# Kernel tuning notes

Hardware: AMD Instinct MI355X
Metric: run time of the kernel (lower is better)

Reference implementation:

```python
import jax, jax.numpy as jnp
import numpy as np

B, S, D = 4, 2048, 1024
H = 4 * D          # expert hidden dim
E_SPEC = 4         # num specific experts
E_SHR = 2          # num shared experts
TOP_K = 2


def setup_inputs() -> dict:
    key = jax.random.key(0)
    ks = jax.random.split(key, 16)
    s = 0.02
    return {
        "x": jax.random.normal(ks[0], (B, S, D), jnp.float32),
        # specific experts (stacked over expert axis)
        "spec_w1": jax.random.normal(ks[1], (E_SPEC, D, H), jnp.float32) * s,
        "spec_b1": jnp.zeros((E_SPEC, H), jnp.float32),
        "spec_w2": jax.random.normal(ks[2], (E_SPEC, H, D), jnp.float32) * s,
        "spec_b2": jnp.zeros((E_SPEC, D), jnp.float32),
        "spec_rw": jax.random.normal(ks[3], (D, E_SPEC), jnp.float32) * s,
        "spec_rb": jnp.zeros((E_SPEC,), jnp.float32),
        # shared experts
        "shr_w1": jax.random.normal(ks[4], (E_SHR, D, H), jnp.float32) * s,
        "shr_b1": jnp.zeros((E_SHR, H), jnp.float32),
        "shr_w2": jax.random.normal(ks[5], (E_SHR, H, D), jnp.float32) * s,
        "shr_b2": jnp.zeros((E_SHR, D), jnp.float32),
        "shr_rw": jax.random.normal(ks[6], (D, E_SHR), jnp.float32) * s,
        "shr_rb": jnp.zeros((E_SHR,), jnp.float32),
    }


def _expert_mlp(xf, w1, b1, w2, b2):
    # xf: [T, D]; w1: [E, D, H]; w2: [E, H, D] -> [E, T, D]
    h = jax.nn.gelu(jnp.einsum("td,edh->eth", xf, w1) + b1[:, None, :],
                    approximate=False)
    return jnp.einsum("eth,ehd->etd", h, w2) + b2[:, None, :]


def reference(x, spec_w1, spec_b1, spec_w2, spec_b2, spec_rw, spec_rb,
              shr_w1, shr_b1, shr_w2, shr_b2, shr_rw, shr_rb):
    b, s, d = x.shape
    xf = x.reshape(-1, d)                      # [T, D]
    T = xf.shape[0]

    # --- specific (top-k) routing ---
    spec_probs = jax.nn.softmax(xf @ spec_rw + spec_rb, axis=-1)   # [T, E]
    topk_probs, topk_idx = jax.lax.top_k(spec_probs, TOP_K)        # [T, K]

    # aux load-balancing loss
    counts = jnp.zeros((E_SPEC,), jnp.float32).at[topk_idx.reshape(-1)].add(1.0)
    fraction = counts / (T * TOP_K)
    aux_loss = E_SPEC * jnp.sum(fraction * spec_probs.mean(axis=0))

    # gate[t, e] = sum_k topk_probs[t,k] * 1[topk_idx[t,k]==e]
    gate = jnp.sum(jax.nn.one_hot(topk_idx, E_SPEC, dtype=xf.dtype)
                   * topk_probs[..., None], axis=1)                # [T, E]

    spec_out_e = _expert_mlp(xf, spec_w1, spec_b1, spec_w2, spec_b2)  # [E, T, D]
    specific_out = jnp.einsum("te,etd->td", gate, spec_out_e)

    # --- shared (dense) experts ---
    shr_probs = jax.nn.softmax(xf @ shr_rw + shr_rb, axis=-1)      # [T, E_shr]
    shr_out_e = _expert_mlp(xf, shr_w1, shr_b1, shr_w2, shr_b2)    # [E_shr, T, D]
    shared_out = jnp.einsum("te,etd->td", shr_probs, shr_out_e)

    final = (specific_out + shared_out).reshape(b, s, d)
    return final, aux_loss
```

## Files before the change

kernel.cpp:

```cpp
#include <hip/hip_runtime.h>
#include <hip/hip_bf16.h>

#define T_TOK 8192
#define DDIM 1024
#define HDIM 4096

typedef __bf16 bf16;
typedef bf16 bf16x8 __attribute__((ext_vector_type(8)));
typedef float f32x4 __attribute__((ext_vector_type(4)));

#define ASM_VMCNT(n) asm volatile("s_waitcnt vmcnt(" #n ")" ::: "memory")
#define MFMA16(a, b, c) __builtin_amdgcn_mfma_f32_16x16x32_bf16((a), (b), (c), 0, 0, 0)

__device__ __forceinline__ void gl_lds16(const void* g, void* l) {
  __builtin_amdgcn_global_load_lds(
      (const __attribute__((address_space(1))) unsigned int*)g,
      (__attribute__((address_space(3))) unsigned int*)l, 16, 0, 0);
}

__device__ __forceinline__ float gelu_f(float v) {
  const float x = v * 0.7071067811865475f;
  const float ax = fabsf(x);
  const float t = 1.0f / fmaf(0.3275911f, ax, 1.0f);
  float p = fmaf(1.061405429f, t, -1.453152027f);
  p = fmaf(p, t, 1.421413741f);
  p = fmaf(p, t, -0.284496736f);
  p = fmaf(p, t, 0.254829592f);
  p = p * t;
  const float e = __expf(-ax * ax);
  const float er = fmaf(-p, e, 1.0f);
  const float erfx = (x >= 0.0f) ? er : -er;
  return 0.5f * v * (1.0f + erfx);
}

__global__ __launch_bounds__(256) void conv_router(
    const float* __restrict__ x, bf16* __restrict__ xb,
    const float* __restrict__ srw, const float* __restrict__ srb,
    const float* __restrict__ hrw, const float* __restrict__ hrb,
    float* __restrict__ gate, float4* __restrict__ probs4,
    int* __restrict__ top2) {
  const int lane = threadIdx.x & 63;
  const int w = threadIdx.x >> 6;
  const int t = blockIdx.x * 4 + w;

  const float* xr = x + (size_t)t * DDIM;
  bf16* xbr = xb + (size_t)t * DDIM;
  float p0 = 0, p1 = 0, p2 = 0, p3 = 0, p4 = 0, p5 = 0;
#pragma unroll
  for (int c = 0; c < 4; ++c) {
    const int d = c * 256 + lane * 4;
    const float4 xv = *(const float4*)(xr + d);
    bf16 ov[4] = {(bf16)xv.x, (bf16)xv.y, (bf16)xv.z, (bf16)xv.w};
    *(float2*)(xbr + d) = *(float2*)ov;
    const float xa[4] = {xv.x, xv.y, xv.z, xv.w};
#pragma unroll
    for (int j = 0; j < 4; ++j) {
      const float xd = xa[j];
      const float4 r4 = *(const float4*)(srw + (size_t)(d + j) * 4);
      p0 += xd * r4.x; p1 += xd * r4.y; p2 += xd * r4.z; p3 += xd * r4.w;
      const float2 r2 = *(const float2*)(hrw + (size_t)(d + j) * 2);
      p4 += xd * r2.x; p5 += xd * r2.y;
    }
  }
#pragma unroll
  for (int off = 32; off >= 1; off >>= 1) {
    p0 += __shfl_xor(p0, off);
    p1 += __shfl_xor(p1, off);
    p2 += __shfl_xor(p2, off);
    p3 += __shfl_xor(p3, off);
    p4 += __shfl_xor(p4, off);
    p5 += __shfl_xor(p5, off);
  }
  if (lane == 0) {
    const float l0 = p0 + srb[0], l1 = p1 + srb[1];
    const float l2 = p2 + srb[2], l3 = p3 + srb[3];
    const float m = fmaxf(fmaxf(l0, l1), fmaxf(l2, l3));
    const float e0 = expf(l0 - m), e1 = expf(l1 - m);
    const float e2 = expf(l2 - m), e3 = expf(l3 - m);
    const float s = e0 + e1 + e2 + e3;
    float pr[4] = {e0 / s, e1 / s, e2 / s, e3 / s};
    int i1 = 0; float v1 = pr[0];
#pragma unroll
    for (int e = 1; e < 4; ++e) if (pr[e] > v1) { v1 = pr[e]; i1 = e; }
    int i2 = -1; float v2 = -1.0f;
#pragma unroll
    for (int e = 0; e < 4; ++e)
      if (e != i1 && pr[e] > v2) { v2 = pr[e]; i2 = e; }
    float g[4] = {0, 0, 0, 0};
    g[i1] = v1; g[i2] = v2;
    float* gr = gate + (size_t)t * 8;
    gr[0] = g[0]; gr[1] = g[1]; gr[2] = g[2]; gr[3] = g[3];
    const float h0 = p4 + hrb[0], h1 = p5 + hrb[1];
    const float mh = fmaxf(h0, h1);
    const float q0 = expf(h0 - mh), q1 = expf(h1 - mh);
    const float qs = q0 + q1;
    gr[4] = q0 / qs; gr[5] = q1 / qs; gr[6] = 0; gr[7] = 0;
    probs4[t] = make_float4(pr[0], pr[1], pr[2], pr[3]);
    top2[t] = i1 | (i2 << 8);
  }
}

__global__ __launch_bounds__(256) void transpose_convert6(
    const float* __restrict__ spec_w, const float* __restrict__ shr_w,
    bf16* __restrict__ dst, int R, int C) {
  __shared__ float tile[32][33];
  const int z = blockIdx.z;
  const float* src = (z < 4) ? spec_w + (size_t)z * R * C
                             : shr_w + (size_t)(z - 4) * R * C;
  bf16* d = dst + (size_t)z * R * C;
  const int c0 = blockIdx.x * 32, r0 = blockIdx.y * 32;
  const int tx = threadIdx.x & 31, ty = threadIdx.x >> 5;
#pragma unroll
  for (int i = 0; i < 4; ++i)
    tile[ty + 8 * i][tx] = src[(size_t)(r0 + ty + 8 * i) * C + c0 + tx];
  __syncthreads();
#pragma unroll
  for (int i = 0; i < 4; ++i)
    d[(size_t)(c0 + ty + 8 * i) * R + r0 + tx] = (bf16)tile[tx][ty + 8 * i];
}

__global__ __launch_bounds__(1024) void scan_build(
    const int* __restrict__ top2, const float4* __restrict__ probs4,
    int* __restrict__ meta, int* __restrict__ lists,
    float* __restrict__ auxg) {
  __shared__ unsigned long long sc[1024];
  __shared__ float4 rp[512];
  const int tid = threadIdx.x;

  int ee[8];
  unsigned long long c = 0;
  float4 ps = make_float4(0.f, 0.f, 0.f, 0.f);
#pragma unroll
  for (int j = 0; j < 8; ++j) {
    const int t = tid * 8 + j;
    const int p = top2[t];
    ee[j] = p;
    const int a = p & 15, b = (p >> 8) & 15;
    c += (1ULL << (16 * a)) + (1ULL << (16 * b));
    const float4 pv = probs4[t];
    ps.x += pv.x; ps.y += pv.y; ps.z += pv.z; ps.w += pv.w;
  }
  sc[tid] = c;
  __syncthreads();
  for (int off = 1; off < 1024; off <<= 1) {
    const unsigned long long mine = sc[tid];
    const unsigned long long prev = (tid >= off) ? sc[tid - off] : 0ULL;
    __syncthreads();
    sc[tid] = mine + prev;
    __syncthreads();
  }
  const unsigned long long incl = sc[tid];
  const unsigned long long tot = sc[1023];
  const unsigned long long excl = incl - c;
  int q0 = (int)(excl & 0xffff), q1 = (int)((excl >> 16) & 0xffff);
  int q2 = (int)((excl >> 32) & 0xffff), q3 = (int)((excl >> 48) & 0xffff);
#pragma unroll
  for (int j = 0; j < 8; ++j) {
    const int t = tid * 8 + j;
    const int a = ee[j] & 15, b = (ee[j] >> 8) & 15;
    const int pa = (a == 0) ? q0 : (a == 1) ? q1 : (a == 2) ? q2 : q3;
    lists[a * 8192 + pa] = t;
    q0 += (a == 0); q1 += (a == 1); q2 += (a == 2); q3 += (a == 3);
    const int pb = (b == 0) ? q0 : (b == 1) ? q1 : (b == 2) ? q2 : q3;
    lists[b * 8192 + pb] = t;
    q0 += (b == 0); q1 += (b == 1); q2 += (b == 2); q3 += (b == 3);
  }
  if (tid == 1023) {
    const int c0 = (int)(tot & 0xffff), c1 = (int)((tot >> 16) & 0xffff);
    const int c2 = (int)((tot >> 32) & 0xffff), c3 = (int)((tot >> 48) & 0xffff);
    meta[24] = c0; meta[25] = c1; meta[26] = c2; meta[27] = c3;
    auxg[0] = (float)c0; auxg[1] = (float)c1;
    auxg[2] = (float)c2; auxg[3] = (float)c3;
    const int nb0 = (c0 + 255) >> 8, nb1 = (c1 + 255) >> 8;
    const int nb2 = (c2 + 255) >> 8, nb3 = (c3 + 255) >> 8;
    const int ch0 = (nb0 + 3) >> 2, ch1 = (nb1 + 3) >> 2;
    const int ch2 = (nb2 + 3) >> 2, ch3 = (nb3 + 3) >> 2;
    meta[28] = 0;
    meta[29] = 128 * ch0;
    meta[30] = meta[29] + 128 * ch1;
    meta[31] = meta[30] + 128 * ch2;
    meta[32] = meta[31] + 128 * ch3;
    meta[34] = 0;
    meta[35] = nb0 * 256;
    meta[36] = meta[35] + nb1 * 256;
    meta[37] = meta[36] + nb2 * 256;
  }
  if (tid >= 512) rp[tid - 512] = ps;
  __syncthreads();
  if (tid < 512) {
    const float4 o = rp[tid];
    ps.x += o.x; ps.y += o.y; ps.z += o.z; ps.w += o.w;
  }
  for (int w = 256; w >= 1; w >>= 1) {
    __syncthreads();
    if (tid >= w && tid < 2 * w) rp[tid - w] = ps;
    __syncthreads();
    if (tid < w) {
      const float4 o = rp[tid];
      ps.x += o.x; ps.y += o.y; ps.z += o.z; ps.w += o.w;
    }
  }
  if (tid == 0) {
    auxg[4] = ps.x; auxg[5] = ps.y; auxg[6] = ps.z; auxg[7] = ps.w;
  }
}

__global__ void aux_finalize(const float* __restrict__ auxg,
                             float* __restrict__ outp) {
  float a = 0.0f;
#pragma unroll
  for (int e = 0; e < 4; ++e)
    a += (auxg[e] / (float)(T_TOK * 2)) * (auxg[4 + e] / (float)T_TOK);
  outp[0] = 4.0f * a;
}

template <int KIND>
__global__ __launch_bounds__(256, 2) void g1k(
    const bf16* __restrict__ A, const bf16* __restrict__ B,
    const float* __restrict__ bias, bf16* __restrict__ h_all, int N,
    int NCN, int CH_M, int CH_N, const int* __restrict__ meta,
    const int* __restrict__ lists, int e) {
  __shared__ __align__(1024) bf16 As[3 * 256 * 32];
  __shared__ __align__(1024) bf16 Bs[3 * 128 * 32];

  const int tid = threadIdx.x;
  const int lane = tid & 63, wid = tid >> 6;
  const int wm = wid >> 1, wn = wid & 1;
  const int lr = lane & 15, lg = lane >> 4;

  int bm, bn, hb = 0, s = e;
  const bf16* Bp = B;
  const float* biasp = bias;
  if constexpr (KIND == 0) {
    const int xcd = blockIdx.x & 7, idx = blockIdx.x >> 3;
    bm = (xcd / NCN) * CH_M + idx / CH_N;
    bn = (xcd % NCN) * CH_N + idx % CH_N;
  } else if constexpr (KIND == 1) {
    const int b = blockIdx.x;
    if (b >= meta[32]) return;
    s = (b >= meta[29]) + (b >= meta[30]) + (b >= meta[31]);
    const int local = b - meta[28 + s];
    const int nbm = (meta[24 + s] + 255) >> 8;
    const int CHm = (nbm + 3) >> 2;
    if (local >= 8 * CHm * 16) return;
    const int xc = local & 7, idx = local >> 3;
    bm = (xc >> 1) * CHm + idx / 16;
    bn = (xc & 1) * 16 + idx % 16;
    if (bm >= nbm) return;
    hb = meta[34 + s];
    Bp = B + (size_t)s * DDIM * HDIM;
    biasp = bias + (size_t)s * HDIM;
  } else {
    const int nbm = (meta[24 + e] + 255) >> 8;
    const int CHm = (nbm + 3) >> 2;
    if (blockIdx.x >= 8 * CHm * 16) return;
    const int xc = blockIdx.x & 7, idx = blockIdx.x >> 3;
    bm = (xc >> 1) * CHm + idx / 16;
    bn = (xc & 1) * 16 + idx % 16;
    if (bm >= nbm) return;
  }
  const int K = DDIM;

  const int rl = tid >> 2;
  const int c = ((tid & 3) * 16) ^ (((rl >> 1) & 3) << 4);
  int ar0 = bm * 256 + rl, ar1 = ar0 + 64, ar2 = ar0 + 128, ar3 = ar0 + 192;
  if constexpr (KIND != 0) {
    const int* lp = lists + s * 8192;
    int t;
    t = lp[ar0]; ar0 = t < 0 ? 0 : t;
    t = lp[ar1]; ar1 = t < 0 ? 0 : t;
    t = lp[ar2]; ar2 = t < 0 ? 0 : t;
    t = lp[ar3]; ar3 = t < 0 ? 0 : t;
  }
  const bf16* sA0 = A + (size_t)ar0 * K + (c >> 1);
  const bf16* sA1 = A + (size_t)ar1 * K + (c >> 1);
  const bf16* sA2 = A + (size_t)ar2 * K + (c >> 1);
  const bf16* sA3 = A + (size_t)ar3 * K + (c >> 1);
  const bf16* sB0 = Bp + (size_t)(bn * 128 + rl) * K + (c >> 1);
  const bf16* sB1 = Bp + (size_t)(bn * 128 + 64 + rl) * K + (c >> 1);

  char* const dA = (char*)As + wid * 1024;
  char* const dB = (char*)Bs + wid * 1024;

  const int rkey = ((lr >> 1) & 3) << 4;
  const char* Ard = (const char*)As + (wm * 128 + lr) * 64 + ((lg * 16) ^ rkey);
  const char* Brd = (const char*)Bs + (wn * 64 + lr) * 64 + ((lg * 16) ^ rkey);

  f32x4 acc[8][4] = {};
  const int NT = K >> 5;

#define GW_STAGE(KO, SLOT)                         \
  gl_lds16(sA0 + (KO), dA + (SLOT)*16384);         \
  gl_lds16(sA1 + (KO), dA + (SLOT)*16384 + 4096);  \
  gl_lds16(sA2 + (KO), dA + (SLOT)*16384 + 8192);  \
  gl_lds16(sA3 + (KO), dA + (SLOT)*16384 + 12288); \
  gl_lds16(sB0 + (KO), dB + (SLOT)*8192);          \
  gl_lds16(sB1 + (KO), dB + (SLOT)*8192 + 4096);
  GW_STAGE(0, 0)
  GW_STAGE(32, 1)
  GW_STAGE(64, 2)
  ASM_VMCNT(12);
  __builtin_amdgcn_s_barrier();

#define GW_ITER(KT, SLOT)                                                  \
  {                                                                        \
    bf16x8 af[8], bfr[4];                                                  \
    _Pragma("unroll") for (int mf = 0; mf < 8; ++mf)                       \
        af[mf] = *(const bf16x8*)(Ard + (SLOT)*16384 + mf * 1024);         \
    _Pragma("unroll") for (int nf = 0; nf < 4; ++nf)                       \
        bfr[nf] = *(const bf16x8*)(Brd + (SLOT)*8192 + nf * 1024);         \
    asm volatile("s_waitcnt lgkmcnt(0)" ::: "memory");                     \
    __builtin_amdgcn_s_setprio(1);                                         \
    _Pragma("unroll") for (int mf = 0; mf < 8; ++mf)                       \
        _Pragma("unroll") for (int nf = 0; nf < 4; ++nf)                   \
            acc[mf][nf] = MFMA16(af[mf], bfr[nf], acc[mf][nf]);            \
    __builtin_amdgcn_s_setprio(0);                                         \
    __builtin_amdgcn_s_barrier();                                          \
    if ((KT) + 3 < NT) {                                                   \
      const int ko_ = ((KT) + 3) << 5;                                     \
      GW_STAGE(ko_, SLOT)                                                  \
      ASM_VMCNT(12);                                                       \
    } else if ((KT) + 2 < NT) {                                            \
      ASM_VMCNT(6);                                                        \
    } else if ((KT) + 1 < NT) {                                            \
      ASM_VMCNT(0);                                                        \
    }                                                                      \
    __builtin_amdgcn_s_barrier();                                          \
  }

  for (int kt0 = 0; kt0 < NT; kt0 += 3) {
    GW_ITER(kt0, 0)
    if (kt0 + 1 < NT) GW_ITER(kt0 + 1, 1)
    if (kt0 + 2 < NT) GW_ITER(kt0 + 2, 2)
  }

  const int colb = bn * 128 + wn * 64;
  const int rowb = hb + bm * 256 + wm * 128 + lg * 4;
  float bv[4];
#pragma unroll
  for (int nf = 0; nf < 4; ++nf) bv[nf] = biasp[colb + nf * 16 + lr];
#pragma unroll
  for (int mf = 0; mf < 8; ++mf)
#pragma unroll
    for (int nf = 0; nf < 4; ++nf) {
      const int col = colb + nf * 16 + lr;
#pragma unroll
      for (int r = 0; r < 4; ++r) {
        const int row = rowb + mf * 16 + r;
        h_all[(size_t)row * N + col] = (bf16)gelu_f(acc[mf][nf][r] + bv[nf]);
      }
    }
}

template <int EMODE>
__global__ __launch_bounds__(512, 2) void g2k(
    const bf16* __restrict__ A, int lda, const bf16* __restrict__ B,
    const float* __restrict__ bias, float* __restrict__ out,
    const float* __restrict__ gate, int gidx, const int* __restrict__ meta,
    const int* __restrict__ lists, int e, int packed) {
  __shared__ __align__(1024) bf16 Alds[2 * 256 * 64];
  __shared__ __align__(1024) bf16 Blds[2 * 128 * 64];

  const int tid = threadIdx.x;
  const int lane = tid & 63, wid = tid >> 6;
  const int wm = wid >> 2, wn = wid & 3;
  const int lr = lane & 15, lg = lane >> 4;

  int bm, bn, hb = 0;
  if constexpr (EMODE == 3) {
    const int nbm = (meta[24 + e] + 255) >> 8;
    const int CHm = (nbm + 3) >> 2;
    if (blockIdx.x >= 8 * CHm * 4) return;
    const int xc = blockIdx.x & 7, idx = blockIdx.x >> 3;
    bm = (xc >> 1) * CHm + idx / 4;
    bn = (xc & 1) * 4 + idx % 4;
    if (bm >= nbm) return;
    hb = packed ? meta[34 + e] : 0;
  } else {
    const int xcd = blockIdx.x & 7, idx = blockIdx.x >> 3;
    bm = (xcd >> 1) * 8 + idx / 4;
    bn = (xcd & 1) * 4 + idx % 4;
  }
  const int K = HDIM, N = DDIM;
  const int NT = K >> 6;

  const int L = tid * 16;
  const int rl = L >> 7;
  const int colb = (L & 127) ^ ((rl & 7) << 4);

  const int ar0 = hb + bm * 256 + rl;
  const bf16* sAc0 = A + (size_t)ar0 * lda + (colb >> 1);
  const bf16* sAc1 = A + (size_t)(ar0 + 64) * lda + (colb >> 1);
  const bf16* sAc2 = A + (size_t)(ar0 + 128) * lda + (colb >> 1);
  const bf16* sAc3 = A + (size_t)(ar0 + 192) * lda + (colb >> 1);
  const bf16* sB = B + (size_t)(bn * 128 + rl) * K + (colb >> 1);

  char* const ldsA = (char*)Alds;
  char* const ldsB = (char*)Blds;
  const int wb = wid * 1024;
  char* const stA[2] = {ldsA + wb, ldsA + 32768 + wb};
  char* const stB[2] = {ldsB + wb, ldsB + 16384 + wb};

  const int ax0 = (lg * 16) ^ ((lr & 7) << 4);
  const int ax1 = ax0 ^ 64;
  const int aro = (wm * 128 + lr) * 128;
  const int bro = (wn * 32 + lr) * 128;
  const char* const Ak0[2] = {ldsA + aro + ax0, ldsA + 32768 + aro + ax0};
  const char* const Ak1[2] = {ldsA + aro + ax1, ldsA + 32768 + aro + ax1};
  const char* const Bk0[2] = {ldsB + bro + ax0, ldsB + 16384 + bro + ax0};
  const char* const Bk1[2] = {ldsB + bro + ax1, ldsB + 16384 + bro + ax1};

  f32x4 acc[8][2] = {};

  gl_lds16(sAc0, stA[0]);
  gl_lds16(sAc1, stA[0] + 8192);
  gl_lds16(sAc2, stA[0] + 16384);
  gl_lds16(sAc3, stA[0] + 24576);
  gl_lds16(sB, stB[0]);
  gl_lds16(sB + (size_t)64 * K, stB[0] + 8192);
  gl_lds16(sB + 64, stB[1]);
  gl_lds16(sB + (size_t)64 * K + 64, stB[1] + 8192);
  gl_lds16(sAc0 + 64, stA[1]);
  gl_lds16(sAc1 + 64, stA[1] + 8192);
  ASM_VMCNT(4);
  __builtin_amdgcn_s_barrier();

  for (int kt0 = 0; kt0 < NT; kt0 += 2) {
#pragma unroll
    for (int par = 0; par < 2; ++par) {
      const int kt = kt0 + par;
      const int cur = par, oth = par ^ 1;
      const bool st1 = (kt + 1) < NT, st2 = (kt + 2) < NT;
      const size_t ko1 = (size_t)(kt + 1) << 6, ko2 = (size_t)(kt + 2) << 6;
      const char* Ac0 = Ak0[cur]; const char* Ac1 = Ak1[cur];
      const char* Bc0 = Bk0[cur]; const char* Bc1 = Bk1[cur];

      bf16x8 af[4][2], bfr[2][2];

#pragma unroll
      for (int mf = 0; mf < 4; ++mf) {
        af[mf][0] = *(const bf16x8*)(Ac0 + mf * 2048);
        af[mf][1] = *(const bf16x8*)(Ac1 + mf * 2048);
      }
      bfr[0][0] = *(const bf16x8*)(Bc0);
      bfr[0][1] = *(const bf16x8*)(Bc1);
      if (st1) {
        gl_lds16(sAc2 + ko1, stA[oth] + 16384);
        gl_lds16(sAc3 + ko1, stA[oth] + 24576);
      }
      __builtin_amdgcn_s_barrier();
      asm volatile("s_waitcnt lgkmcnt(0)" ::: "memory");
      __builtin_amdgcn_sched_barrier(0);
      __builtin_amdgcn_s_setprio(1);
#pragma unroll
      for (int mf = 0; mf < 4; ++mf) {
        acc[mf][0] = MFMA16(af[mf][0], bfr[0][0], acc[mf][0]);
        acc[mf][0] = MFMA16(af[mf][1], bfr[0][1], acc[mf][0]);
      }
      __builtin_amdgcn_s_setprio(0);
      __builtin_amdgcn_s_barrier();

      bfr[1][0] = *(const bf16x8*)(Bc0 + 2048);
      bfr[1][1] = *(const bf16x8*)(Bc1 + 2048);
      __builtin_amdgcn_s_barrier();
      asm volatile("s_waitcnt lgkmcnt(0)" ::: "memory");
      __builtin_amdgcn_sched_barrier(0);
      __builtin_amdgcn_s_setprio(1);
#pragma unroll
      for (int mf = 0; mf < 4; ++mf) {
        acc[mf][1] = MFMA16(af[mf][0], bfr[1][0], acc[mf][1]);
        acc[mf][1] = MFMA16(af[mf][1], bfr[1][1], acc[mf][1]);
      }
      __builtin_amdgcn_s_setprio(0);
      __builtin_amdgcn_s_barrier();

#pragma unroll
      for (int mf = 0; mf < 4; ++mf) {
        af[mf][0] = *(const bf16x8*)(Ac0 + 8192 + mf * 2048);
        af[mf][1] = *(const bf16x8*)(Ac1 + 8192 + mf * 2048);
      }
      if (st2) {
        gl_lds16(sB + ko2, stB[cur]);
        gl_lds16(sB + (size_t)64 * K + ko2, stB[cur] + 8192);
      }
      __builtin_amdgcn_s_barrier();
      asm volatile("s_waitcnt lgkmcnt(0)" ::: "memory");
      __builtin_amdgcn_sched_barrier(0);
      __builtin_amdgcn_s_setprio(1);
#pragma unroll
      for (int mf = 0; mf < 4; ++mf) {
        acc[4 + mf][0] = MFMA16(af[mf][0], bfr[0][0], acc[4 + mf][0]);
        acc[4 + mf][0] = MFMA16(af[mf][1], bfr[0][1], acc[4 + mf][0]);
      }
      __builtin_amdgcn_s_setprio(0);
      __builtin_amdgcn_s_barrier();

      if (st2) {
        gl_lds16(sAc0 + ko2, stA[cur]);
        gl_lds16(sAc1 + ko2, stA[cur] + 8192);
      }
      __builtin_amdgcn_s_setprio(1);
#pragma unroll
      for (int mf = 0; mf < 4; ++mf) {
        acc[4 + mf][1] = MFMA16(af[mf][0], bfr[1][0], acc[4 + mf][1]);
        acc[4 + mf][1] = MFMA16(af[mf][1], bfr[1][1], acc[4 + mf][1]);
      }
      __builtin_amdgcn_s_setprio(0);
      if (st2) {
        ASM_VMCNT(4);
        __builtin_amdgcn_s_barrier();
      } else if (st1) {
        ASM_VMCNT(0);
        __builtin_amdgcn_s_barrier();
      }
    }
  }

  const int colb2 = bn * 128 + wn * 32;
  const int rowb = bm * 256 + wm * 128 + lg * 4;
  float bv[2];
#pragma unroll
  for (int nf = 0; nf < 2; ++nf) bv[nf] = bias[colb2 + nf * 16 + lr];
#pragma unroll
  for (int mf = 0; mf < 8; ++mf) {
    if constexpr (EMODE != 3) {
      float gv[4];
#pragma unroll
      for (int r = 0; r < 4; ++r)
        gv[r] = gate[(size_t)(rowb + mf * 16 + r) * 8 + gidx];
#pragma unroll
      for (int nf = 0; nf < 2; ++nf) {
        const int col = colb2 + nf * 16 + lr;
#pragma unroll
        for (int r = 0; r < 4; ++r) {
          const float v = acc[mf][nf][r] + bv[nf];
          const size_t oi = (size_t)(rowb + mf * 16 + r) * N + col;
          if constexpr (EMODE == 1)
            out[oi] += gv[r] * v;
          else
            out[oi] = gv[r] * v;
        }
      }
    } else {
      const int* lp = lists + e * 8192;
      int tok[4]; float gv[4];
#pragma unroll
      for (int r = 0; r < 4; ++r) {
        tok[r] = lp[rowb + mf * 16 + r];
        gv[r] = tok[r] >= 0 ? gate[(size_t)tok[r] * 8 + gidx] : 0.0f;
      }
#pragma unroll
      for (int nf = 0; nf < 2; ++nf) {
        const int col = colb2 + nf * 16 + lr;
#pragma unroll
        for (int r = 0; r < 4; ++r) {
          if (tok[r] >= 0) {
            const float v = acc[mf][nf][r] + bv[nf];
            out[(size_t)tok[r] * N + col] += gv[r] * v;
          }
        }
      }
    }
  }
}

extern "C" void kernel_launch(void* const* d_in, const int* in_sizes, int n_in,
                              void* d_out, int out_size, void* d_ws,
                              size_t ws_size, hipStream_t stream) {
  const float* x = (const float*)d_in[0];
  const float* spec_w1 = (const float*)d_in[1];
  const float* spec_b1 = (const float*)d_in[2];
  const float* spec_w2 = (const float*)d_in[3];
  const float* spec_b2 = (const float*)d_in[4];
  const float* spec_rw = (const float*)d_in[5];
  const float* spec_rb = (const float*)d_in[6];
  const float* shr_w1 = (const float*)d_in[7];
  const float* shr_b1 = (const float*)d_in[8];
  const float* shr_w2 = (const float*)d_in[9];
  const float* shr_b2 = (const float*)d_in[10];
  const float* shr_rw = (const float*)d_in[11];
  const float* shr_rb = (const float*)d_in[12];
  float* out = (float*)d_out;

  char* ws = (char*)d_ws;
  const size_t DH = (size_t)DDIM * HDIM;
  const size_t OFF_W1 = 16777216;
  const size_t OFF_W2 = OFF_W1 + 50331648;
  const size_t OFF_GATE = OFF_W2 + 50331648;
  const size_t OFF_AUX = OFF_GATE + 262144;
  const size_t OFF_META = OFF_AUX + 256;
  const size_t OFF_LIST = OFF_META + 256;
  const size_t OFF_T2 = OFF_LIST + 131072;
  const size_t OFF_P4 = OFF_T2 + 32768;
  const size_t OFF_H = OFF_P4 + 131072 + 1024;
  bf16* xb = (bf16*)ws;
  bf16* w1t = (bf16*)(ws + OFF_W1);
  bf16* w2t = (bf16*)(ws + OFF_W2);
  float* gate = (float*)(ws + OFF_GATE);
  float* auxg = (float*)(ws + OFF_AUX);
  int* meta = (int*)(ws + OFF_META);
  int* lists = (int*)(ws + OFF_LIST);
  int* top2 = (int*)(ws + OFF_T2);
  float4* probs4 = (float4*)(ws + OFF_P4);
  bf16* h = (bf16*)(ws + OFF_H);

  const bool rich = ws_size >= OFF_H + (size_t)17408 * HDIM * 2;

  hipMemsetAsync(lists, 0xFF, 4 * 8192 * 4, stream);

  conv_router<<<T_TOK / 4, 256, 0, stream>>>(x, xb, spec_rw, spec_rb, shr_rw,
                                             shr_rb, gate, probs4, top2);
  scan_build<<<1, 1024, 0, stream>>>(top2, probs4, meta, lists, auxg);

  transpose_convert6<<<dim3(HDIM / 32, DDIM / 32, 6), 256, 0, stream>>>(
      spec_w1, shr_w1, w1t, DDIM, HDIM);
  transpose_convert6<<<dim3(DDIM / 32, HDIM / 32, 6), 256, 0, stream>>>(
      spec_w2, shr_w2, w2t, HDIM, DDIM);

  if (rich) {
    g1k<0><<<2048, 256, 0, stream>>>(xb, w1t + 4 * DH, shr_b1, h, 8192,
                                     4, 16, 16, meta, lists, 0);
    g2k<0><<<256, 512, 0, stream>>>(h, 8192, w2t + 4 * DH, shr_b2, out,
                                    gate, 4, meta, lists, 0, 0);
    g2k<1><<<256, 512, 0, stream>>>(h + 4096, 8192, w2t + 5 * DH,
                                    shr_b2 + 1024, out, gate, 5, meta,
                                    lists, 0, 0);
    g1k<1><<<4096, 256, 0, stream>>>(xb, w1t, spec_b1, h, 4096,
                                     2, 8, 16, meta, lists, 0);
    for (int e = 0; e < 4; ++e)
      g2k<3><<<256, 512, 0, stream>>>(h, 4096, w2t + (size_t)e * DH,
                                      spec_b2 + (size_t)e * DDIM, out, gate,
                                      e, meta, lists, e, 1);
  } else {
    for (int es = 0; es < 2; ++es) {
      g1k<0><<<1024, 256, 0, stream>>>(xb, w1t + (4 + es) * DH,
                                       shr_b1 + (size_t)es * HDIM, h, 4096,
                                       2, 8, 16, meta, lists, 0);
      if (es == 0)
        g2k<0><<<256, 512, 0, stream>>>(h, 4096, w2t + 4 * DH, shr_b2, out,
                                        gate, 4, meta, lists, 0, 0);
      else
        g2k<1><<<256, 512, 0, stream>>>(h, 4096, w2t + 5 * DH,
                                        shr_b2 + 1024, out, gate, 5, meta,
                                        lists, 0, 0);
    }
    for (int e = 0; e < 4; ++e) {
      g1k<2><<<1024, 256, 0, stream>>>(xb, w1t + (size_t)e * DH,
                                       spec_b1 + (size_t)e * HDIM, h, 4096,
                                       2, 8, 16, meta, lists, e);
      g2k<3><<<256, 512, 0, stream>>>(h, 4096, w2t + (size_t)e * DH,
                                      spec_b2 + (size_t)e * DDIM, out, gate,
                                      e, meta, lists, e, 0);
    }
  }
  aux_finalize<<<1, 1, 0, stream>>>(auxg, out + (size_t)T_TOK * DDIM);
}
```

Baseline: 1.019 ms.

## Replace first-layer GEMM with 256x256 tile, 8-wave, ping-pong pipelined kernel

The first expert GEMM kernel moves from a 256x128 tile with 4 waves and a 3-stage K=32 pipeline to a 256x256 tile with 8 waves, K=64 steps and two LDS buffers. Global-to-LDS loads are interleaved with MFMA phases under fine-grained barriers, and the LDS swizzle and block-to-XCD mapping are updated to match. The aim is higher arithmetic intensity per loaded byte and better overlap of loads with matrix math. The cost is larger LDS use (128 KB per block), which limits occupancy, plus many extra barriers per K step. Grid sizes and routing metadata offsets are rescaled for the new tile width.

```diff
diff --git a/kernel.cpp b/kernel.cpp
--- a/kernel.cpp
+++ b/kernel.cpp
@@ -11,6 +11,10 @@
 
 #define ASM_VMCNT(n) asm volatile("s_waitcnt vmcnt(" #n ")" ::: "memory")
 #define MFMA16(a, b, c) __builtin_amdgcn_mfma_f32_16x16x32_bf16((a), (b), (c), 0, 0, 0)
+#define G8_BAR __builtin_amdgcn_s_barrier()
+#define G8_WAIT                                            \
+  asm volatile("s_waitcnt lgkmcnt(0)" ::: "memory");       \
+  __builtin_amdgcn_sched_barrier(0)
 
 __device__ __forceinline__ void gl_lds16(const void* g, void* l) {
   __builtin_amdgcn_global_load_lds(
@@ -175,15 +179,15 @@
     const int nb2 = (c2 + 255) >> 8, nb3 = (c3 + 255) >> 8;
     const int ch0 = (nb0 + 3) >> 2, ch1 = (nb1 + 3) >> 2;
     const int ch2 = (nb2 + 3) >> 2, ch3 = (nb3 + 3) >> 2;
-    meta[28] = 0;
-    meta[29] = 128 * ch0;
-    meta[30] = meta[29] + 128 * ch1;
-    meta[31] = meta[30] + 128 * ch2;
-    meta[32] = meta[31] + 128 * ch3;
     meta[34] = 0;
     meta[35] = nb0 * 256;
     meta[36] = meta[35] + nb1 * 256;
     meta[37] = meta[36] + nb2 * 256;
+    meta[40] = 0;
+    meta[41] = 64 * ch0;
+    meta[42] = meta[41] + 64 * ch1;
+    meta[43] = meta[42] + 64 * ch2;
+    meta[44] = meta[43] + 64 * ch3;
   }
   if (tid >= 512) rp[tid - 512] = ps;
   __syncthreads();
@@ -215,126 +219,172 @@
 }
 
 template <int KIND>
-__global__ __launch_bounds__(256, 2) void g1k(
-    const bf16* __restrict__ A, const bf16* __restrict__ B,
+__global__ __launch_bounds__(512, 2) void g8(
+    const bf16* __restrict__ A, const bf16* __restrict__ Bw,
     const float* __restrict__ bias, bf16* __restrict__ h_all, int N,
-    int NCN, int CH_M, int CH_N, const int* __restrict__ meta,
+    int CH_M, int CH_N, const int* __restrict__ meta,
     const int* __restrict__ lists, int e) {
-  __shared__ __align__(1024) bf16 As[3 * 256 * 32];
-  __shared__ __align__(1024) bf16 Bs[3 * 128 * 32];
+  __shared__ __align__(1024) bf16 Alds[2 * 256 * 64];
+  __shared__ __align__(1024) bf16 Blds[2 * 256 * 64];
 
   const int tid = threadIdx.x;
   const int lane = tid & 63, wid = tid >> 6;
-  const int wm = wid >> 1, wn = wid & 1;
+  const int wm = wid >> 2, wn = wid & 3;
   const int lr = lane & 15, lg = lane >> 4;
 
   int bm, bn, hb = 0, s = e;
-  const bf16* Bp = B;
+  const bf16* Bp = Bw;
   const float* biasp = bias;
   if constexpr (KIND == 0) {
     const int xcd = blockIdx.x & 7, idx = blockIdx.x >> 3;
-    bm = (xcd / NCN) * CH_M + idx / CH_N;
-    bn = (xcd % NCN) * CH_N + idx % CH_N;
+    bm = (xcd >> 1) * CH_M + idx / CH_N;
+    bn = (xcd & 1) * CH_N + idx % CH_N;
   } else if constexpr (KIND == 1) {
     const int b = blockIdx.x;
-    if (b >= meta[32]) return;
-    s = (b >= meta[29]) + (b >= meta[30]) + (b >= meta[31]);
-    const int local = b - meta[28 + s];
+    if (b >= meta[44]) return;
+    s = (b >= meta[41]) + (b >= meta[42]) + (b >= meta[43]);
+    const int local = b - meta[40 + s];
     const int nbm = (meta[24 + s] + 255) >> 8;
     const int CHm = (nbm + 3) >> 2;
-    if (local >= 8 * CHm * 16) return;
+    if (local >= 64 * CHm) return;
     const int xc = local & 7, idx = local >> 3;
-    bm = (xc >> 1) * CHm + idx / 16;
-    bn = (xc & 1) * 16 + idx % 16;
+    bm = (xc >> 1) * CHm + idx / 8;
+    bn = (xc & 1) * 8 + idx % 8;
     if (bm >= nbm) return;
     hb = meta[34 + s];
-    Bp = B + (size_t)s * DDIM * HDIM;
+    Bp = Bw + (size_t)s * DDIM * HDIM;
     biasp = bias + (size_t)s * HDIM;
   } else {
     const int nbm = (meta[24 + e] + 255) >> 8;
     const int CHm = (nbm + 3) >> 2;
-    if (blockIdx.x >= 8 * CHm * 16) return;
+    if (blockIdx.x >= 64 * CHm) return;
     const int xc = blockIdx.x & 7, idx = blockIdx.x >> 3;
-    bm = (xc >> 1) * CHm + idx / 16;
-    bn = (xc & 1) * 16 + idx % 16;
+    bm = (xc >> 1) * CHm + idx / 8;
+    bn = (xc & 1) * 8 + idx % 8;
     if (bm >= nbm) return;
   }
   const int K = DDIM;
-
-  const int rl = tid >> 2;
-  const int c = ((tid & 3) * 16) ^ (((rl >> 1) & 3) << 4);
-  int ar0 = bm * 256 + rl, ar1 = ar0 + 64, ar2 = ar0 + 128, ar3 = ar0 + 192;
+  const int NT = K >> 6;
+
+  const int rl = tid >> 3;
+  const int cbs = ((tid * 16) & 127) ^ ((rl & 7) << 4);
+  int ar[4];
+#pragma unroll
+  for (int c = 0; c < 4; ++c) ar[c] = bm * 256 + c * 64 + rl;
   if constexpr (KIND != 0) {
     const int* lp = lists + s * 8192;
-    int t;
-    t = lp[ar0]; ar0 = t < 0 ? 0 : t;
-    t = lp[ar1]; ar1 = t < 0 ? 0 : t;
-    t = lp[ar2]; ar2 = t < 0 ? 0 : t;
-    t = lp[ar3]; ar3 = t < 0 ? 0 : t;
-  }
-  const bf16* sA0 = A + (size_t)ar0 * K + (c >> 1);
-  const bf16* sA1 = A + (size_t)ar1 * K + (c >> 1);
-  const bf16* sA2 = A + (size_t)ar2 * K + (c >> 1);
-  const bf16* sA3 = A + (size_t)ar3 * K + (c >> 1);
-  const bf16* sB0 = Bp + (size_t)(bn * 128 + rl) * K + (c >> 1);
-  const bf16* sB1 = Bp + (size_t)(bn * 128 + 64 + rl) * K + (c >> 1);
-
-  char* const dA = (char*)As + wid * 1024;
-  char* const dB = (char*)Bs + wid * 1024;
-
-  const int rkey = ((lr >> 1) & 3) << 4;
-  const char* Ard = (const char*)As + (wm * 128 + lr) * 64 + ((lg * 16) ^ rkey);
-  const char* Brd = (const char*)Bs + (wn * 64 + lr) * 64 + ((lg * 16) ^ rkey);
+#pragma unroll
+    for (int c = 0; c < 4; ++c) {
+      const int t = lp[ar[c]];
+      ar[c] = t < 0 ? 0 : t;
+    }
+  }
+  const bf16* sA[4];
+  const bf16* sB[4];
+#pragma unroll
+  for (int c = 0; c < 4; ++c) {
+    sA[c] = A + (size_t)ar[c] * K + (cbs >> 1);
+    sB[c] = Bp + (size_t)(bn * 256 + c * 64 + rl) * K + (cbs >> 1);
+  }
+  char* const ldsA = (char*)Alds;
+  char* const ldsB = (char*)Blds;
+  const int wb = wid * 1024;
+
+  const int ax0 = (lg * 16) ^ ((lr & 7) << 4);
+  const int ax1 = ax0 ^ 64;
+  const int aro = (wm * 128 + lr) * 128;
+  const int bro = (wn * 64 + lr) * 128;
+  const char* const A0 = (const char*)Alds + aro + ax0;
+  const char* const A1 = (const char*)Alds + aro + ax1;
+  const char* const B0 = (const char*)Blds + bro + ax0;
+  const char* const B1 = (const char*)Blds + bro + ax1;
 
   f32x4 acc[8][4] = {};
-  const int NT = K >> 5;
-
-#define GW_STAGE(KO, SLOT)                         \
-  gl_lds16(sA0 + (KO), dA + (SLOT)*16384);         \
-  gl_lds16(sA1 + (KO), dA + (SLOT)*16384 + 4096);  \
-  gl_lds16(sA2 + (KO), dA + (SLOT)*16384 + 8192);  \
-  gl_lds16(sA3 + (KO), dA + (SLOT)*16384 + 12288); \
-  gl_lds16(sB0 + (KO), dB + (SLOT)*8192);          \
-  gl_lds16(sB1 + (KO), dB + (SLOT)*8192 + 4096);
-  GW_STAGE(0, 0)
-  GW_STAGE(32, 1)
-  GW_STAGE(64, 2)
-  ASM_VMCNT(12);
-  __builtin_amdgcn_s_barrier();
-
-#define GW_ITER(KT, SLOT)                                                  \
-  {                                                                        \
-    bf16x8 af[8], bfr[4];                                                  \
-    _Pragma("unroll") for (int mf = 0; mf < 8; ++mf)                       \
-        af[mf] = *(const bf16x8*)(Ard + (SLOT)*16384 + mf * 1024);         \
-    _Pragma("unroll") for (int nf = 0; nf < 4; ++nf)                       \
-        bfr[nf] = *(const bf16x8*)(Brd + (SLOT)*8192 + nf * 1024);         \
-    asm volatile("s_waitcnt lgkmcnt(0)" ::: "memory");                     \
-    __builtin_amdgcn_s_setprio(1);                                         \
-    _Pragma("unroll") for (int mf = 0; mf < 8; ++mf)                       \
-        _Pragma("unroll") for (int nf = 0; nf < 4; ++nf)                   \
-            acc[mf][nf] = MFMA16(af[mf], bfr[nf], acc[mf][nf]);            \
-    __builtin_amdgcn_s_setprio(0);                                         \
-    __builtin_amdgcn_s_barrier();                                          \
-    if ((KT) + 3 < NT) {                                                   \
-      const int ko_ = ((KT) + 3) << 5;                                     \
-      GW_STAGE(ko_, SLOT)                                                  \
-      ASM_VMCNT(12);                                                       \
-    } else if ((KT) + 2 < NT) {                                            \
-      ASM_VMCNT(6);                                                        \
-    } else if ((KT) + 1 < NT) {                                            \
-      ASM_VMCNT(0);                                                        \
-    }                                                                      \
-    __builtin_amdgcn_s_barrier();                                          \
-  }
-
-  for (int kt0 = 0; kt0 < NT; kt0 += 3) {
-    GW_ITER(kt0, 0)
-    if (kt0 + 1 < NT) GW_ITER(kt0 + 1, 1)
-    if (kt0 + 2 < NT) GW_ITER(kt0 + 2, 2)
-  }
-
-  const int colb = bn * 128 + wn * 64;
+  bf16x8 af[4][2], b01[2][2], b23[2][2];
+
+#define G8_RA(BOFF, MB)                                               \
+  _Pragma("unroll") for (int i = 0; i < 4; ++i) {                     \
+    af[i][0] = *(const bf16x8*)(A0 + (BOFF) + ((MB) + i) * 2048);     \
+    af[i][1] = *(const bf16x8*)(A1 + (BOFF) + ((MB) + i) * 2048);     \
+  }
+#define G8_RB(BOFF, DST, NB)                                          \
+  _Pragma("unroll") for (int i = 0; i < 2; ++i) {                     \
+    DST[i][0] = *(const bf16x8*)(B0 + (BOFF) + ((NB) + i) * 2048);    \
+    DST[i][1] = *(const bf16x8*)(B1 + (BOFF) + ((NB) + i) * 2048);    \
+  }
+#define G8_MMA(MB, NB, BSRC)                                          \
+  __builtin_amdgcn_s_setprio(1);                                      \
+  _Pragma("unroll") for (int i = 0; i < 4; ++i)                       \
+    _Pragma("unroll") for (int j = 0; j < 2; ++j) {                   \
+      acc[(MB) + i][(NB) + j] =                                       \
+          MFMA16(af[i][0], BSRC[j][0], acc[(MB) + i][(NB) + j]);      \
+      acc[(MB) + i][(NB) + j] =                                       \
+          MFMA16(af[i][1], BSRC[j][1], acc[(MB) + i][(NB) + j]);      \
+    }                                                                 \
+  __builtin_amdgcn_s_setprio(0);
+#define G8_STG_B(T, C, BUFO)                                          \
+  gl_lds16(sB[C] + (size_t)(T) * 64, ldsB + (BUFO) + (C) * 8192 + wb);
+#define G8_STG_A(T, C, BUFO)                                          \
+  gl_lds16(sA[C] + (size_t)(T) * 64, ldsA + (BUFO) + (C) * 8192 + wb);
+
+  G8_STG_B(0, 0, 0) G8_STG_B(0, 1, 0) G8_STG_B(0, 2, 0) G8_STG_B(0, 3, 0)
+  G8_STG_A(0, 0, 0) G8_STG_A(0, 1, 0) G8_STG_A(0, 2, 0) G8_STG_A(0, 3, 0)
+  G8_STG_B(1, 0, 32768) G8_STG_B(1, 1, 32768)
+  G8_STG_B(1, 2, 32768) G8_STG_B(1, 3, 32768)
+  G8_STG_A(1, 0, 32768) G8_STG_A(1, 1, 32768)
+  G8_STG_A(1, 2, 32768) G8_STG_A(1, 3, 32768)
+  ASM_VMCNT(8);
+  G8_BAR;
+
+  for (int t = 0; t < NT; t += 2) {
+    const bool stg = (t + 2) < NT;
+    G8_RA(0, 0);
+    G8_RB(0, b01, 0);
+    G8_BAR; G8_WAIT;
+    G8_MMA(0, 0, b01);
+    G8_BAR;
+    G8_RB(0, b23, 2);
+    G8_BAR; G8_WAIT;
+    G8_MMA(0, 2, b23);
+    G8_BAR;
+    G8_RA(0, 4);
+    if (stg) { G8_STG_B(t + 2, 0, 0) G8_STG_B(t + 2, 1, 0) }
+    G8_BAR; G8_WAIT;
+    G8_MMA(4, 0, b01);
+    G8_BAR;
+    if (stg) { G8_STG_B(t + 2, 2, 0) G8_STG_B(t + 2, 3, 0) }
+    G8_MMA(4, 2, b23);
+    if (stg) ASM_VMCNT(4); else ASM_VMCNT(0);
+    G8_BAR;
+    G8_RA(32768, 0);
+    G8_RB(32768, b01, 0);
+    if (stg) { G8_STG_A(t + 2, 0, 0) G8_STG_A(t + 2, 1, 0) }
+    G8_BAR; G8_WAIT;
+    G8_MMA(0, 0, b01);
+    G8_BAR;
+    G8_RB(32768, b23, 2);
+    if (stg) { G8_STG_A(t + 2, 2, 0) G8_STG_A(t + 2, 3, 0) }
+    G8_BAR; G8_WAIT;
+    G8_MMA(0, 2, b23);
+    G8_BAR;
+    G8_RA(32768, 4);
+    if (stg) {
+      G8_STG_B(t + 3, 0, 32768) G8_STG_B(t + 3, 1, 32768)
+      G8_STG_B(t + 3, 2, 32768) G8_STG_B(t + 3, 3, 32768)
+    }
+    G8_BAR; G8_WAIT;
+    G8_MMA(4, 0, b01);
+    G8_BAR;
+    if (stg) {
+      G8_STG_A(t + 3, 0, 32768) G8_STG_A(t + 3, 1, 32768)
+      G8_STG_A(t + 3, 2, 32768) G8_STG_A(t + 3, 3, 32768)
+    }
+    G8_MMA(4, 2, b23);
+    if (stg) ASM_VMCNT(8);
+    G8_BAR;
+  }
+
+  const int colb = bn * 256 + wn * 64;
   const int rowb = hb + bm * 256 + wm * 128 + lg * 4;
   float bv[4];
 #pragma unroll
@@ -618,24 +668,24 @@
       spec_w2, shr_w2, w2t, HDIM, DDIM);
 
   if (rich) {
-    g1k<0><<<2048, 256, 0, stream>>>(xb, w1t + 4 * DH, shr_b1, h, 8192,
-                                     4, 16, 16, meta, lists, 0);
+    g8<0><<<1024, 512, 0, stream>>>(xb, w1t + 4 * DH, shr_b1, h, 8192,
+                                    8, 16, meta, lists, 0);
     g2k<0><<<256, 512, 0, stream>>>(h, 8192, w2t + 4 * DH, shr_b2, out,
                                     gate, 4, meta, lists, 0, 0);
     g2k<1><<<256, 512, 0, stream>>>(h + 4096, 8192, w2t + 5 * DH,
                                     shr_b2 + 1024, out, gate, 5, meta,
                                     lists, 0, 0);
-    g1k<1><<<4096, 256, 0, stream>>>(xb, w1t, spec_b1, h, 4096,
-                                     2, 8, 16, meta, lists, 0);
+    g8<1><<<2048, 512, 0, stream>>>(xb, w1t, spec_b1, h, 4096,
+                                    0, 8, meta, lists, 0);
     for (int e = 0; e < 4; ++e)
       g2k<3><<<256, 512, 0, stream>>>(h, 4096, w2t + (size_t)e * DH,
                                       spec_b2 + (size_t)e * DDIM, out, gate,
                                       e, meta, lists, e, 1);
   } else {
     for (int es = 0; es < 2; ++es) {
-      g1k<0><<<1024, 256, 0, stream>>>(xb, w1t + (4 + es) * DH,
-                                       shr_b1 + (size_t)es * HDIM, h, 4096,
-                                       2, 8, 16, meta, lists, 0);
+      g8<0><<<512, 512, 0, stream>>>(xb, w1t + (4 + es) * DH,
+                                     shr_b1 + (size_t)es * HDIM, h, 4096,
+                                     8, 8, meta, lists, 0);
       if (es == 0)
         g2k<0><<<256, 512, 0, stream>>>(h, 4096, w2t + 4 * DH, shr_b2, out,
                                         gate, 4, meta, lists, 0, 0);
@@ -645,9 +695,9 @@
                                         lists, 0, 0);
     }
     for (int e = 0; e < 4; ++e) {
-      g1k<2><<<1024, 256, 0, stream>>>(xb, w1t + (size_t)e * DH,
-                                       spec_b1 + (size_t)e * HDIM, h, 4096,
-                                       2, 8, 16, meta, lists, e);
+      g8<2><<<512, 512, 0, stream>>>(xb, w1t + (size_t)e * DH,
+                                     spec_b1 + (size_t)e * HDIM, h, 4096,
+                                     0, 8, meta, lists, e);
       g2k<3><<<256, 512, 0, stream>>>(h, 4096, w2t + (size_t)e * DH,
                                       spec_b2 + (size_t)e * DDIM, out, gate,
                                       e, meta, lists, e, 0);
```

New measurement: 1.016 ms. No clear change (-0.4%).
